# Kernel optimization log

Hardware: AMD Instinct MI355X
Metric: run time of the kernel (lower is better)

## Reference

```python
import jax, jax.numpy as jnp
import numpy as np

D_MODEL = 256
N_HEAD = 8


def quick_gelu(x):
    return x * jax.nn.sigmoid(1.702 * x)


def setup_inputs() -> dict:
    key = jax.random.key(0)
    ks = jax.random.split(key, 7)
    d = D_MODEL
    s = 0.02
    return {
        "x": jax.random.normal(ks[0], (2, 512, d), dtype=jnp.float32),
        "W_qkv": jax.random.normal(ks[1], (d, 3 * d), dtype=jnp.float32) * s,
        "b_qkv": jnp.zeros((3 * d,), dtype=jnp.float32),
        "W_fc": jax.random.normal(ks[2], (d, 4 * d), dtype=jnp.float32) * s,
        "b_fc": jnp.zeros((4 * d,), dtype=jnp.float32),
        "W_proj": jax.random.normal(ks[3], (4 * d, d), dtype=jnp.float32) * s,
        "b_proj": jnp.zeros((d,), dtype=jnp.float32),
    }


def attention_l1(x, W_qkv, b_qkv):
    bs, n_ctx, width = x.shape
    h = N_HEAD
    c = width // h
    scale = 1.0 / jnp.sqrt(jnp.asarray(c, x.dtype))
    qkv = (x @ W_qkv + b_qkv).reshape(bs, n_ctx, h, 3 * c)
    q, k, v = jnp.split(qkv, 3, axis=-1)  # each (b, t, h, c)
    qh = q.transpose(0, 2, 1, 3)  # (b, h, t, c)
    kh = k.transpose(0, 2, 1, 3)  # (b, h, s, c)
    vh = v.transpose(0, 2, 1, 3)  # (b, h, s, c)
    # L1 distance: sum_c |q - k| * scale  -> (b, h, t, s)
    dist = jnp.sum(jnp.abs(qh[:, :, :, None, :] - kh[:, :, None, :, :]), axis=-1) * scale
    weight = 1.0 / (0.001 + dist)
    idx = jnp.arange(n_ctx)
    weight = weight.at[:, :, idx, idx].set(0.0)
    wdtype = weight.dtype
    weight = jax.nn.softmax(weight.astype(jnp.float32), axis=-1).astype(wdtype)
    out = jnp.einsum('bhts,bhsc->bthc', weight, vh)
    return out.reshape(bs, n_ctx, width)


def reference(x, W_qkv, b_qkv, W_fc, b_fc, W_proj, b_proj):
    x = x + attention_l1(x, W_qkv, b_qkv)
    h = quick_gelu(x @ W_fc + b_fc)
    x = x + (h @ W_proj + b_proj)
    return x
```

## Files before the change

kernel.cpp:

```cpp
#include <hip/hip_runtime.h>
#include <hip/hip_bf16.h>

#define DM   256
#define NH   8
#define HC   32
#define SEQ  512
#define BATCH 2
#define MTOT (BATCH*SEQ)

#define OFF_Q    0
#define OFF_K    262144
#define OFF_X1   524288
#define FP32_END 786432
#define BOFF_XB     0
#define BOFF_X1B    262144
#define BOFF_HB     524288
#define BOFF_VTB    1572864
#define BOFF_WQKVT  1835008
#define BOFF_WFCT   2031616
#define BOFF_WPROJT 2293760

typedef __attribute__((ext_vector_type(8))) __bf16 bf16x8;
typedef __attribute__((ext_vector_type(4))) __bf16 bf16x4;
typedef __attribute__((ext_vector_type(4))) float  f32x4;

__device__ __forceinline__ float qgelu(float x) {
    return x / (1.0f + __expf(-1.702f * x));
}

__device__ __forceinline__ void conv_copy(const float* __restrict__ in,
                                          __bf16* __restrict__ out,
                                          int total, int gid) {
    int o = gid * 4;
    if (o >= total) return;
    float4 v = *(const float4*)(in + o);
    bf16x4 b;
    b.x = (__bf16)v.x; b.y = (__bf16)v.y; b.z = (__bf16)v.z; b.w = (__bf16)v.w;
    *(bf16x4*)(out + o) = b;
}

__device__ __forceinline__ void conv_transpose(const float* __restrict__ in,
                                               __bf16* __restrict__ out,
                                               int K, int N, int gid) {
    int o = gid * 4;
    if (o >= K * N) return;
    int n = o / K;
    int k = o - n * K;
    bf16x4 b;
    b.x = (__bf16)in[(size_t)(k + 0) * N + n];
    b.y = (__bf16)in[(size_t)(k + 1) * N + n];
    b.z = (__bf16)in[(size_t)(k + 2) * N + n];
    b.w = (__bf16)in[(size_t)(k + 3) * N + n];
    *(bf16x4*)(out + o) = b;
}

__global__ __launch_bounds__(256)
void convert_k(const float* __restrict__ x,
               const float* __restrict__ Wqkv,
               const float* __restrict__ Wfc,
               const float* __restrict__ Wproj,
               __bf16* __restrict__ wsb)
{
    const int gid = blockIdx.x * 256 + threadIdx.x;
    switch (blockIdx.y) {
        case 0: conv_copy(x, wsb + BOFF_XB, MTOT * DM, gid); break;
        case 1: conv_transpose(Wqkv,  wsb + BOFF_WQKVT,  256, 768,  gid); break;
        case 2: conv_transpose(Wfc,   wsb + BOFF_WFCT,   256, 1024, gid); break;
        case 3: conv_transpose(Wproj, wsb + BOFF_WPROJT, 1024, 256, gid); break;
    }
}

template<int MODE, int K_>
__global__ __launch_bounds__(256)
void mfma_gemm(const __bf16* __restrict__ A, const __bf16* __restrict__ Bt,
               const float* __restrict__ bias, const float* __restrict__ X1res,
               float* __restrict__ Of, __bf16* __restrict__ Ob,
               float* __restrict__ ws, __bf16* __restrict__ vtb, int N)
{
    const int lane = threadIdx.x & 63;
    const int wv   = threadIdx.x >> 6;
    const int m0   = blockIdx.y * 16;
    const int n0   = blockIdx.x * 64 + wv * 16;
    const int r    = lane & 15;
    const int q    = lane >> 4;

    const __bf16* ap = A  + (size_t)(m0 + r) * K_ + q * 8;
    const __bf16* bp = Bt + (size_t)(n0 + r) * K_ + q * 8;

    f32x4 acc = {0.f, 0.f, 0.f, 0.f};
    #pragma unroll
    for (int kt = 0; kt < K_; kt += 32) {
        bf16x8 af = *(const bf16x8*)(ap + kt);
        bf16x8 bf = *(const bf16x8*)(bp + kt);
        acc = __builtin_amdgcn_mfma_f32_16x16x32_bf16(af, bf, acc, 0, 0, 0);
    }

    const int n = n0 + r;
    const float bn = bias[n];
    #pragma unroll
    for (int i = 0; i < 4; ++i) {
        const int m = m0 + q * 4 + i;
        float v = acc[i] + bn;
        if (MODE == 0) {
            const int b  = m >> 9, t = m & 511;
            const int h  = n / 96, jj = n % 96;
            const int bh = b * NH + h;
            if (jj < 32)      ws[OFF_Q + ((size_t)(bh * SEQ + t)) * HC + jj]        = v;
            else if (jj < 64) ws[OFF_K + ((size_t)(bh * SEQ + t)) * HC + (jj - 32)] = v;
            else              vtb[((size_t)(bh * HC + (jj - 64))) * SEQ + t] = (__bf16)v;
        } else if (MODE == 1) {
            Ob[(size_t)m * N + n] = (__bf16)qgelu(v);
        } else {
            Of[(size_t)m * N + n] = X1res[(size_t)m * N + n] + v;
        }
    }
}

#define QT 16
#define PSTRIDE 514

__global__ __launch_bounds__(512, 4)
void attn_k(const float* __restrict__ wq, const float* __restrict__ wk,
            const __bf16* __restrict__ vtb, const float* __restrict__ xin,
            float* __restrict__ x1, __bf16* __restrict__ x1b)
{
    __shared__ float  qtile[QT * 32];
    __shared__ __bf16 pmat[QT * PSTRIDE];
    __shared__ float  psum[QT * 8];
    __shared__ float  pinv[QT];

    const int tid  = threadIdx.x;
    const int lane = tid & 63;
    const int wv   = tid >> 6;
    const int sg   = tid;
    const int bh   = blockIdx.x >> 5;
    const int qbase = (blockIdx.x & 31) * QT;
    const float scale = 0.17677669529663687f;

    const float* krow = wk + ((size_t)(bh * SEQ + sg)) * HC;
    float kr[32];
    #pragma unroll
    for (int j = 0; j < 8; ++j) {
        float4 k4 = *(const float4*)&krow[j * 4];
        kr[j*4+0] = k4.x; kr[j*4+1] = k4.y; kr[j*4+2] = k4.z; kr[j*4+3] = k4.w;
    }
    if (tid < QT * 32 / 4) {
        *(float4*)&qtile[tid * 4] =
            *(const float4*)&wq[((size_t)(bh * SEQ + qbase)) * HC + tid * 4];
    }
    __syncthreads();

    #pragma unroll 4
    for (int t = 0; t < QT; ++t) {
        float d = 0.f;
        #pragma unroll
        for (int j = 0; j < 8; ++j) {
            float4 q4 = *(const float4*)&qtile[t * 32 + j * 4];
            d += fabsf(kr[j*4+0] - q4.x) + fabsf(kr[j*4+1] - q4.y)
               + fabsf(kr[j*4+2] - q4.z) + fabsf(kr[j*4+3] - q4.w);
        }
        float w = 1.0f / (0.001f + d * scale);
        if (sg == qbase + t) w = 0.0f;
        float p = __expf(w);
        float se = p;
        #pragma unroll
        for (int off = 32; off >= 1; off >>= 1) se += __shfl_xor(se, off, 64);
        pmat[t * PSTRIDE + sg] = (__bf16)p;
        if (lane == 0) psum[t * 8 + wv] = se;
    }
    __syncthreads();

    if (tid < QT) {
        float s = 0.f;
        #pragma unroll
        for (int j = 0; j < 8; ++j) s += psum[tid * 8 + j];
        pinv[tid] = 1.0f / s;
    }
    __syncthreads();

    if (wv < 2) {
        const int r = lane & 15, q = lane >> 4;
        const __bf16* bp  = vtb + ((size_t)(bh * HC + wv * 16 + r)) * SEQ + q * 8;
        const __bf16* apm = &pmat[r * PSTRIDE + q * 8];

        f32x4 acc = {0.f, 0.f, 0.f, 0.f};
        #pragma unroll
        for (int kt = 0; kt < SEQ; kt += 32) {
            bf16x8 af = *(const bf16x8*)(apm + kt);
            bf16x8 bf = *(const bf16x8*)(bp + kt);
            acc = __builtin_amdgcn_mfma_f32_16x16x32_bf16(af, bf, acc, 0, 0, 0);
        }

        const int b = bh >> 3, hh = bh & 7;
        const int c = wv * 16 + r;
        #pragma unroll
        for (int i = 0; i < 4; ++i) {
            const int tl = q * 4 + i;
            const int t  = qbase + tl;
            const float v = acc[i] * pinv[tl];
            const int idx = ((b * SEQ + t) * DM) + hh * HC + c;
            const float res = xin[idx] + v;
            x1[idx]  = res;
            x1b[idx] = (__bf16)res;
        }
    }
}

extern "C" void kernel_launch(void* const* d_in, const int* in_sizes, int n_in,
                              void* d_out, int out_size, void* d_ws, size_t ws_size,
                              hipStream_t stream)
{
    (void)in_sizes; (void)n_in; (void)out_size; (void)ws_size;
    const float* x     = (const float*)d_in[0];
    const float* Wqkv  = (const float*)d_in[1];
    const float* bqkv  = (const float*)d_in[2];
    const float* Wfc   = (const float*)d_in[3];
    const float* bfc   = (const float*)d_in[4];
    const float* Wproj = (const float*)d_in[5];
    const float* bproj = (const float*)d_in[6];
    float* out = (float*)d_out;
    float* ws  = (float*)d_ws;
    __bf16* wsb = (__bf16*)(ws + FP32_END);

    convert_k<<<dim3(256, 4), 256, 0, stream>>>(x, Wqkv, Wfc, Wproj, wsb);

    mfma_gemm<0, 256><<<dim3(768/64, MTOT/16), 256, 0, stream>>>(
        wsb + BOFF_XB, wsb + BOFF_WQKVT, bqkv, nullptr,
        nullptr, nullptr, ws, wsb + BOFF_VTB, 768);

    attn_k<<<dim3(512), 512, 0, stream>>>(
        ws + OFF_Q, ws + OFF_K, wsb + BOFF_VTB, x, ws + OFF_X1, wsb + BOFF_X1B);

    mfma_gemm<1, 256><<<dim3(1024/64, MTOT/16), 256, 0, stream>>>(
        wsb + BOFF_X1B, wsb + BOFF_WFCT, bfc, nullptr,
        nullptr, wsb + BOFF_HB, ws, nullptr, 1024);

    mfma_gemm<2, 1024><<<dim3(256/64, MTOT/16), 256, 0, stream>>>(
        wsb + BOFF_HB, wsb + BOFF_WPROJT, bproj, ws + OFF_X1,
        out, nullptr, ws, nullptr, 256);
}
```

Baseline: 116.8 us.

## Fuse all stages into one cooperative persistent kernel with grid syncs

Replaces the five separate launches (convert, QKV GEMM, attention, FC GEMM, proj GEMM) with a single cooperative kernel of 256 blocks of 1024 threads, separated by grid.sync barriers. Weight transposes now go through an LDS tile for coalesced access. Attention processes 32 query rows per block. The proj GEMM is split along K into four parts and reduced in LDS. This removes launch gaps and tail effects at the cost of grid-wide barriers and a fixed grid size, which may limit occupancy.

```diff
diff --git a/kernel.cpp b/kernel.cpp
--- a/kernel.cpp
+++ b/kernel.cpp
@@ -1,12 +1,14 @@
 #include <hip/hip_runtime.h>
 #include <hip/hip_bf16.h>
+#include <hip/hip_cooperative_groups.h>
+
+namespace cg = cooperative_groups;
 
 #define DM   256
 #define NH   8
 #define HC   32
 #define SEQ  512
-#define BATCH 2
-#define MTOT (BATCH*SEQ)
+#define MTOT 1024
 
 #define OFF_Q    0
 #define OFF_K    262144
@@ -24,69 +26,23 @@
 typedef __attribute__((ext_vector_type(4))) __bf16 bf16x4;
 typedef __attribute__((ext_vector_type(4))) float  f32x4;
 
+#define QT 32
+#define PSTRIDE 514
+
 __device__ __forceinline__ float qgelu(float x) {
     return x / (1.0f + __expf(-1.702f * x));
 }
 
-__device__ __forceinline__ void conv_copy(const float* __restrict__ in,
-                                          __bf16* __restrict__ out,
-                                          int total, int gid) {
-    int o = gid * 4;
-    if (o >= total) return;
-    float4 v = *(const float4*)(in + o);
-    bf16x4 b;
-    b.x = (__bf16)v.x; b.y = (__bf16)v.y; b.z = (__bf16)v.z; b.w = (__bf16)v.w;
-    *(bf16x4*)(out + o) = b;
-}
-
-__device__ __forceinline__ void conv_transpose(const float* __restrict__ in,
-                                               __bf16* __restrict__ out,
-                                               int K, int N, int gid) {
-    int o = gid * 4;
-    if (o >= K * N) return;
-    int n = o / K;
-    int k = o - n * K;
-    bf16x4 b;
-    b.x = (__bf16)in[(size_t)(k + 0) * N + n];
-    b.y = (__bf16)in[(size_t)(k + 1) * N + n];
-    b.z = (__bf16)in[(size_t)(k + 2) * N + n];
-    b.w = (__bf16)in[(size_t)(k + 3) * N + n];
-    *(bf16x4*)(out + o) = b;
-}
-
-__global__ __launch_bounds__(256)
-void convert_k(const float* __restrict__ x,
-               const float* __restrict__ Wqkv,
-               const float* __restrict__ Wfc,
-               const float* __restrict__ Wproj,
-               __bf16* __restrict__ wsb)
+template<int MODE, int K_>
+__device__ __forceinline__ void gemm_tile16(
+    const __bf16* __restrict__ A, const __bf16* __restrict__ Bt,
+    const float* __restrict__ bias,
+    __bf16* __restrict__ Ob, float* __restrict__ ws, __bf16* __restrict__ vtb,
+    int m0, int n0, int N, int lane)
 {
-    const int gid = blockIdx.x * 256 + threadIdx.x;
-    switch (blockIdx.y) {
-        case 0: conv_copy(x, wsb + BOFF_XB, MTOT * DM, gid); break;
-        case 1: conv_transpose(Wqkv,  wsb + BOFF_WQKVT,  256, 768,  gid); break;
-        case 2: conv_transpose(Wfc,   wsb + BOFF_WFCT,   256, 1024, gid); break;
-        case 3: conv_transpose(Wproj, wsb + BOFF_WPROJT, 1024, 256, gid); break;
-    }
-}
-
-template<int MODE, int K_>
-__global__ __launch_bounds__(256)
-void mfma_gemm(const __bf16* __restrict__ A, const __bf16* __restrict__ Bt,
-               const float* __restrict__ bias, const float* __restrict__ X1res,
-               float* __restrict__ Of, __bf16* __restrict__ Ob,
-               float* __restrict__ ws, __bf16* __restrict__ vtb, int N)
-{
-    const int lane = threadIdx.x & 63;
-    const int wv   = threadIdx.x >> 6;
-    const int m0   = blockIdx.y * 16;
-    const int n0   = blockIdx.x * 64 + wv * 16;
-    const int r    = lane & 15;
-    const int q    = lane >> 4;
-
+    const int r = lane & 15, q = lane >> 4;
     const __bf16* ap = A  + (size_t)(m0 + r) * K_ + q * 8;
     const __bf16* bp = Bt + (size_t)(n0 + r) * K_ + q * 8;
-
     f32x4 acc = {0.f, 0.f, 0.f, 0.f};
     #pragma unroll
     for (int kt = 0; kt < K_; kt += 32) {
@@ -94,7 +50,6 @@
         bf16x8 bf = *(const bf16x8*)(bp + kt);
         acc = __builtin_amdgcn_mfma_f32_16x16x32_bf16(af, bf, acc, 0, 0, 0);
     }
-
     const int n = n0 + r;
     const float bn = bias[n];
     #pragma unroll
@@ -108,100 +63,190 @@
             if (jj < 32)      ws[OFF_Q + ((size_t)(bh * SEQ + t)) * HC + jj]        = v;
             else if (jj < 64) ws[OFF_K + ((size_t)(bh * SEQ + t)) * HC + (jj - 32)] = v;
             else              vtb[((size_t)(bh * HC + (jj - 64))) * SEQ + t] = (__bf16)v;
-        } else if (MODE == 1) {
+        } else {
             Ob[(size_t)m * N + n] = (__bf16)qgelu(v);
-        } else {
-            Of[(size_t)m * N + n] = X1res[(size_t)m * N + n] + v;
-        }
-    }
-}
-
-#define QT 16
-#define PSTRIDE 514
-
-__global__ __launch_bounds__(512, 4)
-void attn_k(const float* __restrict__ wq, const float* __restrict__ wk,
-            const __bf16* __restrict__ vtb, const float* __restrict__ xin,
-            float* __restrict__ x1, __bf16* __restrict__ x1b)
+        }
+    }
+}
+
+__global__ __launch_bounds__(1024, 4)
+void fused_k(const float* __restrict__ x,
+             const float* __restrict__ Wqkv, const float* __restrict__ bqkv,
+             const float* __restrict__ Wfc,  const float* __restrict__ bfc,
+             const float* __restrict__ Wproj,const float* __restrict__ bproj,
+             float* __restrict__ out, float* __restrict__ ws)
 {
-    __shared__ float  qtile[QT * 32];
-    __shared__ __bf16 pmat[QT * PSTRIDE];
-    __shared__ float  psum[QT * 8];
-    __shared__ float  pinv[QT];
-
+    __shared__ __align__(16) float smem[9600];
+    __bf16* wsb = (__bf16*)(ws + FP32_END);
     const int tid  = threadIdx.x;
+    const int bid  = blockIdx.x;
     const int lane = tid & 63;
     const int wv   = tid >> 6;
-    const int sg   = tid;
-    const int bh   = blockIdx.x >> 5;
-    const int qbase = (blockIdx.x & 31) * QT;
-    const float scale = 0.17677669529663687f;
-
-    const float* krow = wk + ((size_t)(bh * SEQ + sg)) * HC;
-    float kr[32];
-    #pragma unroll
-    for (int j = 0; j < 8; ++j) {
-        float4 k4 = *(const float4*)&krow[j * 4];
-        kr[j*4+0] = k4.x; kr[j*4+1] = k4.y; kr[j*4+2] = k4.z; kr[j*4+3] = k4.w;
-    }
-    if (tid < QT * 32 / 4) {
-        *(float4*)&qtile[tid * 4] =
-            *(const float4*)&wq[((size_t)(bh * SEQ + qbase)) * HC + tid * 4];
-    }
-    __syncthreads();
-
-    #pragma unroll 4
-    for (int t = 0; t < QT; ++t) {
-        float d = 0.f;
+    cg::grid_group grid = cg::this_grid();
+
+    if (bid >= 176) {
+        int gid = (bid - 176) * 1024 + tid;
+        if (gid < MTOT * DM / 4) {
+            float4 v = *(const float4*)(x + gid * 4);
+            bf16x4 b;
+            b.x = (__bf16)v.x; b.y = (__bf16)v.y; b.z = (__bf16)v.z; b.w = (__bf16)v.w;
+            *(bf16x4*)(wsb + BOFF_XB + gid * 4) = b;
+        }
+    } else {
+        const float* src; __bf16* dst; int K, N, tile;
+        if (bid < 48)       { src = Wqkv;  dst = wsb + BOFF_WQKVT;  K = 256;  N = 768;  tile = bid; }
+        else if (bid < 112) { src = Wfc;   dst = wsb + BOFF_WFCT;   K = 256;  N = 1024; tile = bid - 48; }
+        else                { src = Wproj; dst = wsb + BOFF_WPROJT; K = 1024; N = 256;  tile = bid - 112; }
+        const int nn = N >> 6;
+        const int k0 = (tile / nn) * 64, n0 = (tile % nn) * 64;
+        float* lt = smem;
+        const int rr = tid >> 4, c4 = tid & 15;
+        float4 v = *(const float4*)&src[(size_t)(k0 + rr) * N + n0 + c4 * 4];
+        lt[rr * 65 + c4 * 4 + 0] = v.x; lt[rr * 65 + c4 * 4 + 1] = v.y;
+        lt[rr * 65 + c4 * 4 + 2] = v.z; lt[rr * 65 + c4 * 4 + 3] = v.w;
+        __syncthreads();
+        bf16x4 b;
+        b.x = (__bf16)lt[(c4 * 4 + 0) * 65 + rr];
+        b.y = (__bf16)lt[(c4 * 4 + 1) * 65 + rr];
+        b.z = (__bf16)lt[(c4 * 4 + 2) * 65 + rr];
+        b.w = (__bf16)lt[(c4 * 4 + 3) * 65 + rr];
+        *(bf16x4*)&dst[(size_t)(n0 + rr) * K + k0 + c4 * 4] = b;
+    }
+    grid.sync();
+
+    {
+        const int widx = bid * 16 + wv;
+        if (widx < 3072) {
+            const int mt = widx & 63, nt = widx >> 6;
+            gemm_tile16<0, 256>(wsb + BOFF_XB, wsb + BOFF_WQKVT, bqkv,
+                                nullptr, ws, wsb + BOFF_VTB,
+                                mt * 16, nt * 16, 768, lane);
+        }
+    }
+    grid.sync();
+
+    {
+        float*  qtile = smem;
+        __bf16* pmat  = (__bf16*)(smem + 1024);
+        float*  psum  = smem + 1024 + (QT * PSTRIDE) / 2;
+        float*  pinv  = psum + QT * 8;
+        const int bh    = bid >> 4;
+        const int qbase = (bid & 15) * QT;
+        const int hf    = tid >> 9;
+        const int sg    = tid & 511;
+        const float scale = 0.17677669529663687f;
+
+        const float* krow = ws + OFF_K + ((size_t)(bh * SEQ + sg)) * HC;
+        float kr[32];
         #pragma unroll
         for (int j = 0; j < 8; ++j) {
-            float4 q4 = *(const float4*)&qtile[t * 32 + j * 4];
-            d += fabsf(kr[j*4+0] - q4.x) + fabsf(kr[j*4+1] - q4.y)
-               + fabsf(kr[j*4+2] - q4.z) + fabsf(kr[j*4+3] - q4.w);
-        }
-        float w = 1.0f / (0.001f + d * scale);
-        if (sg == qbase + t) w = 0.0f;
-        float p = __expf(w);
-        float se = p;
-        #pragma unroll
-        for (int off = 32; off >= 1; off >>= 1) se += __shfl_xor(se, off, 64);
-        pmat[t * PSTRIDE + sg] = (__bf16)p;
-        if (lane == 0) psum[t * 8 + wv] = se;
-    }
-    __syncthreads();
-
-    if (tid < QT) {
-        float s = 0.f;
-        #pragma unroll
-        for (int j = 0; j < 8; ++j) s += psum[tid * 8 + j];
-        pinv[tid] = 1.0f / s;
-    }
-    __syncthreads();
-
-    if (wv < 2) {
+            float4 k4 = *(const float4*)&krow[j * 4];
+            kr[j*4+0] = k4.x; kr[j*4+1] = k4.y; kr[j*4+2] = k4.z; kr[j*4+3] = k4.w;
+        }
+        if (tid < 256) {
+            *(float4*)&qtile[tid * 4] =
+                *(const float4*)&ws[OFF_Q + ((size_t)(bh * SEQ + qbase)) * HC + tid * 4];
+        }
+        __syncthreads();
+
+        #pragma unroll 4
+        for (int tl = 0; tl < 16; ++tl) {
+            const int trow = hf * 16 + tl;
+            float d = 0.f;
+            #pragma unroll
+            for (int j = 0; j < 8; ++j) {
+                float4 q4 = *(const float4*)&qtile[trow * 32 + j * 4];
+                d += fabsf(kr[j*4+0] - q4.x) + fabsf(kr[j*4+1] - q4.y)
+                   + fabsf(kr[j*4+2] - q4.z) + fabsf(kr[j*4+3] - q4.w);
+            }
+            float w = 1.0f / (0.001f + d * scale);
+            if (sg == qbase + trow) w = 0.0f;
+            float p = __expf(w);
+            float se = p;
+            #pragma unroll
+            for (int off = 32; off >= 1; off >>= 1) se += __shfl_xor(se, off, 64);
+            pmat[trow * PSTRIDE + sg] = (__bf16)p;
+            if (lane == 0) psum[trow * 8 + (wv & 7)] = se;
+        }
+        __syncthreads();
+        if (tid < QT) {
+            float s = 0.f;
+            #pragma unroll
+            for (int j = 0; j < 8; ++j) s += psum[tid * 8 + j];
+            pinv[tid] = 1.0f / s;
+        }
+        __syncthreads();
+
+        if (wv < 4) {
+            const int r = lane & 15, q = lane >> 4;
+            const int qtl = wv >> 1, ctl = wv & 1;
+            const __bf16* apm = &pmat[(qtl * 16 + r) * PSTRIDE + q * 8];
+            const __bf16* bp  = wsb + BOFF_VTB +
+                                ((size_t)(bh * HC + ctl * 16 + r)) * SEQ + q * 8;
+            f32x4 acc = {0.f, 0.f, 0.f, 0.f};
+            #pragma unroll
+            for (int kt = 0; kt < SEQ; kt += 32) {
+                bf16x8 af = *(const bf16x8*)(apm + kt);
+                bf16x8 bf = *(const bf16x8*)(bp + kt);
+                acc = __builtin_amdgcn_mfma_f32_16x16x32_bf16(af, bf, acc, 0, 0, 0);
+            }
+            const int b = bh >> 3, hh = bh & 7;
+            const int c = ctl * 16 + r;
+            #pragma unroll
+            for (int i = 0; i < 4; ++i) {
+                const int trow = qtl * 16 + q * 4 + i;
+                const int t    = qbase + trow;
+                const float v  = acc[i] * pinv[trow];
+                const int idx  = ((b * SEQ + t) * DM) + hh * HC + c;
+                const float res = x[idx] + v;
+                ws[OFF_X1 + idx]    = res;
+                wsb[BOFF_X1B + idx] = (__bf16)res;
+            }
+        }
+    }
+    grid.sync();
+
+    {
+        const int widx = bid * 16 + wv;
+        const int mt = widx & 63, nt = widx >> 6;
+        gemm_tile16<1, 256>(wsb + BOFF_X1B, wsb + BOFF_WFCT, bfc,
+                            wsb + BOFF_HB, ws, nullptr,
+                            mt * 16, nt * 16, 1024, lane);
+    }
+    grid.sync();
+
+    {
+        float* ared = smem;
+        const int widx = bid * 16 + wv;
+        const int tile = widx >> 2, ks = widx & 3;
+        const int m0 = (tile & 63) * 16, n0 = (tile >> 6) * 16;
         const int r = lane & 15, q = lane >> 4;
-        const __bf16* bp  = vtb + ((size_t)(bh * HC + wv * 16 + r)) * SEQ + q * 8;
-        const __bf16* apm = &pmat[r * PSTRIDE + q * 8];
-
+        const __bf16* ap = wsb + BOFF_HB     + (size_t)(m0 + r) * 1024 + ks * 256 + q * 8;
+        const __bf16* bp = wsb + BOFF_WPROJT + (size_t)(n0 + r) * 1024 + ks * 256 + q * 8;
         f32x4 acc = {0.f, 0.f, 0.f, 0.f};
         #pragma unroll
-        for (int kt = 0; kt < SEQ; kt += 32) {
-            bf16x8 af = *(const bf16x8*)(apm + kt);
-            bf16x8 bf = *(const bf16x8*)(bp + kt);
+        for (int kk = 0; kk < 8; ++kk) {
+            bf16x8 af = *(const bf16x8*)(ap + kk * 32);
+            bf16x8 bf = *(const bf16x8*)(bp + kk * 32);
             acc = __builtin_amdgcn_mfma_f32_16x16x32_bf16(af, bf, acc, 0, 0, 0);
         }
-
-        const int b = bh >> 3, hh = bh & 7;
-        const int c = wv * 16 + r;
-        #pragma unroll
-        for (int i = 0; i < 4; ++i) {
-            const int tl = q * 4 + i;
-            const int t  = qbase + tl;
-            const float v = acc[i] * pinv[tl];
-            const int idx = ((b * SEQ + t) * DM) + hh * HC + c;
-            const float res = xin[idx] + v;
-            x1[idx]  = res;
-            x1b[idx] = (__bf16)res;
+        *(f32x4*)&ared[(wv * 64 + lane) * 4] = acc;
+        __syncthreads();
+        if (wv < 4) {
+            const int tile2 = bid * 4 + wv;
+            const int m0b = (tile2 & 63) * 16, n0b = (tile2 >> 6) * 16;
+            f32x4 a0 = *(const f32x4*)&ared[((wv * 4 + 0) * 64 + lane) * 4];
+            f32x4 a1 = *(const f32x4*)&ared[((wv * 4 + 1) * 64 + lane) * 4];
+            f32x4 a2 = *(const f32x4*)&ared[((wv * 4 + 2) * 64 + lane) * 4];
+            f32x4 a3 = *(const f32x4*)&ared[((wv * 4 + 3) * 64 + lane) * 4];
+            const int n = n0b + r;
+            const float bn = bproj[n];
+            #pragma unroll
+            for (int i = 0; i < 4; ++i) {
+                const int m = m0b + q * 4 + i;
+                const float v = a0[i] + a1[i] + a2[i] + a3[i] + bn;
+                out[(size_t)m * DM + n] = ws[OFF_X1 + (size_t)m * DM + n] + v;
+            }
         }
     }
 }
@@ -220,22 +265,10 @@
     const float* bproj = (const float*)d_in[6];
     float* out = (float*)d_out;
     float* ws  = (float*)d_ws;
-    __bf16* wsb = (__bf16*)(ws + FP32_END);
-
-    convert_k<<<dim3(256, 4), 256, 0, stream>>>(x, Wqkv, Wfc, Wproj, wsb);
-
-    mfma_gemm<0, 256><<<dim3(768/64, MTOT/16), 256, 0, stream>>>(
-        wsb + BOFF_XB, wsb + BOFF_WQKVT, bqkv, nullptr,
-        nullptr, nullptr, ws, wsb + BOFF_VTB, 768);
-
-    attn_k<<<dim3(512), 512, 0, stream>>>(
-        ws + OFF_Q, ws + OFF_K, wsb + BOFF_VTB, x, ws + OFF_X1, wsb + BOFF_X1B);
-
-    mfma_gemm<1, 256><<<dim3(1024/64, MTOT/16), 256, 0, stream>>>(
-        wsb + BOFF_X1B, wsb + BOFF_WFCT, bfc, nullptr,
-        nullptr, wsb + BOFF_HB, ws, nullptr, 1024);
-
-    mfma_gemm<2, 1024><<<dim3(256/64, MTOT/16), 256, 0, stream>>>(
-        wsb + BOFF_HB, wsb + BOFF_WPROJT, bproj, ws + OFF_X1,
-        out, nullptr, ws, nullptr, 256);
-}
+
+    void* args[] = { (void*)&x, (void*)&Wqkv, (void*)&bqkv, (void*)&Wfc,
+                     (void*)&bfc, (void*)&Wproj, (void*)&bproj,
+                     (void*)&out, (void*)&ws };
+    hipLaunchCooperativeKernel((const void*)fused_k, dim3(256), dim3(1024),
+                               args, 0, stream);
+}
```

New measurement: 256.3 us. 2.2x slower.

## Restructure GEMM kernels: LDS-tiled weight transpose, fused x conversion, split-K projection

Applied to the files above, without the earlier changes.

Replaces the strided-gather weight conversion with an LDS-tiled transpose kernel that reads and writes coalesced. The x fp32-to-bf16 copy is folded into the QKV GEMM, which now converts on load. The GEMMs get their own kernels with a one-wave-per-16x16-tile mapping, ordered so that consecutive waves share B rows. The projection GEMM (K=1024) is split into four K slices across waves and reduced through LDS, giving more blocks and shorter serial MFMA chains. The cost is an extra LDS reduction and sync in the projection kernel.

```diff
diff --git a/kernel.cpp b/kernel.cpp
--- a/kernel.cpp
+++ b/kernel.cpp
@@ -5,14 +5,12 @@
 #define NH   8
 #define HC   32
 #define SEQ  512
-#define BATCH 2
-#define MTOT (BATCH*SEQ)
+#define MTOT 1024
 
 #define OFF_Q    0
 #define OFF_K    262144
 #define OFF_X1   524288
 #define FP32_END 786432
-#define BOFF_XB     0
 #define BOFF_X1B    262144
 #define BOFF_HB     524288
 #define BOFF_VTB    1572864
@@ -28,91 +26,76 @@
     return x / (1.0f + __expf(-1.702f * x));
 }
 
-__device__ __forceinline__ void conv_copy(const float* __restrict__ in,
-                                          __bf16* __restrict__ out,
-                                          int total, int gid) {
-    int o = gid * 4;
-    if (o >= total) return;
-    float4 v = *(const float4*)(in + o);
-    bf16x4 b;
-    b.x = (__bf16)v.x; b.y = (__bf16)v.y; b.z = (__bf16)v.z; b.w = (__bf16)v.w;
-    *(bf16x4*)(out + o) = b;
-}
-
-__device__ __forceinline__ void conv_transpose(const float* __restrict__ in,
-                                               __bf16* __restrict__ out,
-                                               int K, int N, int gid) {
-    int o = gid * 4;
-    if (o >= K * N) return;
-    int n = o / K;
-    int k = o - n * K;
-    bf16x4 b;
-    b.x = (__bf16)in[(size_t)(k + 0) * N + n];
-    b.y = (__bf16)in[(size_t)(k + 1) * N + n];
-    b.z = (__bf16)in[(size_t)(k + 2) * N + n];
-    b.w = (__bf16)in[(size_t)(k + 3) * N + n];
-    *(bf16x4*)(out + o) = b;
-}
-
-__global__ __launch_bounds__(256)
-void convert_k(const float* __restrict__ x,
-               const float* __restrict__ Wqkv,
-               const float* __restrict__ Wfc,
-               const float* __restrict__ Wproj,
-               __bf16* __restrict__ wsb)
-{
-    const int gid = blockIdx.x * 256 + threadIdx.x;
-    switch (blockIdx.y) {
-        case 0: conv_copy(x, wsb + BOFF_XB, MTOT * DM, gid); break;
-        case 1: conv_transpose(Wqkv,  wsb + BOFF_WQKVT,  256, 768,  gid); break;
-        case 2: conv_transpose(Wfc,   wsb + BOFF_WFCT,   256, 1024, gid); break;
-        case 3: conv_transpose(Wproj, wsb + BOFF_WPROJT, 1024, 256, gid); break;
-    }
-}
-
-template<int MODE, int K_>
-__global__ __launch_bounds__(256)
-void mfma_gemm(const __bf16* __restrict__ A, const __bf16* __restrict__ Bt,
-               const float* __restrict__ bias, const float* __restrict__ X1res,
-               float* __restrict__ Of, __bf16* __restrict__ Ob,
-               float* __restrict__ ws, __bf16* __restrict__ vtb, int N)
-{
-    const int lane = threadIdx.x & 63;
-    const int wv   = threadIdx.x >> 6;
-    const int m0   = blockIdx.y * 16;
-    const int n0   = blockIdx.x * 64 + wv * 16;
-    const int r    = lane & 15;
-    const int q    = lane >> 4;
-
-    const __bf16* ap = A  + (size_t)(m0 + r) * K_ + q * 8;
-    const __bf16* bp = Bt + (size_t)(n0 + r) * K_ + q * 8;
+__global__ __launch_bounds__(256)
+void trans_k(const float* __restrict__ Wqkv, const float* __restrict__ Wfc,
+             const float* __restrict__ Wproj, __bf16* __restrict__ wsb)
+{
+    __shared__ float lt[64 * 65];
+    const int bid = blockIdx.x, tid = threadIdx.x;
+    const float* src; __bf16* dst; int K, N, tile;
+    if (bid < 48)       { src = Wqkv;  dst = wsb + BOFF_WQKVT;  K = 256;  N = 768;  tile = bid; }
+    else if (bid < 112) { src = Wfc;   dst = wsb + BOFF_WFCT;   K = 256;  N = 1024; tile = bid - 48; }
+    else                { src = Wproj; dst = wsb + BOFF_WPROJT; K = 1024; N = 256;  tile = bid - 112; }
+    const int nn = N >> 6;
+    const int k0 = (tile / nn) * 64, n0 = (tile % nn) * 64;
+    const int rr0 = tid >> 4, c4 = tid & 15;
+    #pragma unroll
+    for (int i = 0; i < 4; ++i) {
+        const int rr = rr0 + i * 16;
+        float4 v = *(const float4*)&src[(size_t)(k0 + rr) * N + n0 + c4 * 4];
+        lt[rr * 65 + c4 * 4 + 0] = v.x; lt[rr * 65 + c4 * 4 + 1] = v.y;
+        lt[rr * 65 + c4 * 4 + 2] = v.z; lt[rr * 65 + c4 * 4 + 3] = v.w;
+    }
+    __syncthreads();
+    #pragma unroll
+    for (int i = 0; i < 4; ++i) {
+        const int rr = rr0 + i * 16;
+        bf16x4 b;
+        b.x = (__bf16)lt[(c4 * 4 + 0) * 65 + rr];
+        b.y = (__bf16)lt[(c4 * 4 + 1) * 65 + rr];
+        b.z = (__bf16)lt[(c4 * 4 + 2) * 65 + rr];
+        b.w = (__bf16)lt[(c4 * 4 + 3) * 65 + rr];
+        *(bf16x4*)&dst[(size_t)(n0 + rr) * K + k0 + c4 * 4] = b;
+    }
+}
+
+__global__ __launch_bounds__(256)
+void qkv_k(const float* __restrict__ x, const __bf16* __restrict__ Bt,
+           const float* __restrict__ bias, float* __restrict__ ws,
+           __bf16* __restrict__ vtb)
+{
+    const int lane = threadIdx.x & 63, wv = threadIdx.x >> 6;
+    const int widx = blockIdx.x * 4 + wv;
+    const int m0 = (widx & 63) * 16, n0 = (widx >> 6) * 16;
+    const int r = lane & 15, q = lane >> 4;
+
+    const float*  ap = x  + (size_t)(m0 + r) * DM + q * 8;
+    const __bf16* bp = Bt + (size_t)(n0 + r) * DM + q * 8;
 
     f32x4 acc = {0.f, 0.f, 0.f, 0.f};
     #pragma unroll
-    for (int kt = 0; kt < K_; kt += 32) {
-        bf16x8 af = *(const bf16x8*)(ap + kt);
+    for (int kt = 0; kt < DM; kt += 32) {
+        float4 a0 = *(const float4*)(ap + kt);
+        float4 a1 = *(const float4*)(ap + kt + 4);
+        bf16x8 af;
+        af[0] = (__bf16)a0.x; af[1] = (__bf16)a0.y; af[2] = (__bf16)a0.z; af[3] = (__bf16)a0.w;
+        af[4] = (__bf16)a1.x; af[5] = (__bf16)a1.y; af[6] = (__bf16)a1.z; af[7] = (__bf16)a1.w;
         bf16x8 bf = *(const bf16x8*)(bp + kt);
         acc = __builtin_amdgcn_mfma_f32_16x16x32_bf16(af, bf, acc, 0, 0, 0);
     }
 
     const int n = n0 + r;
     const float bn = bias[n];
+    const int h = n / 96, jj = n % 96;
     #pragma unroll
     for (int i = 0; i < 4; ++i) {
         const int m = m0 + q * 4 + i;
-        float v = acc[i] + bn;
-        if (MODE == 0) {
-            const int b  = m >> 9, t = m & 511;
-            const int h  = n / 96, jj = n % 96;
-            const int bh = b * NH + h;
-            if (jj < 32)      ws[OFF_Q + ((size_t)(bh * SEQ + t)) * HC + jj]        = v;
-            else if (jj < 64) ws[OFF_K + ((size_t)(bh * SEQ + t)) * HC + (jj - 32)] = v;
-            else              vtb[((size_t)(bh * HC + (jj - 64))) * SEQ + t] = (__bf16)v;
-        } else if (MODE == 1) {
-            Ob[(size_t)m * N + n] = (__bf16)qgelu(v);
-        } else {
-            Of[(size_t)m * N + n] = X1res[(size_t)m * N + n] + v;
-        }
+        const float v = acc[i] + bn;
+        const int b = m >> 9, t = m & 511;
+        const int bh = b * NH + h;
+        if (jj < 32)      ws[OFF_Q + ((size_t)(bh * SEQ + t)) * HC + jj]        = v;
+        else if (jj < 64) ws[OFF_K + ((size_t)(bh * SEQ + t)) * HC + (jj - 32)] = v;
+        else              vtb[((size_t)(bh * HC + (jj - 64))) * SEQ + t] = (__bf16)v;
     }
 }
 
@@ -182,7 +165,6 @@
         const int r = lane & 15, q = lane >> 4;
         const __bf16* bp  = vtb + ((size_t)(bh * HC + wv * 16 + r)) * SEQ + q * 8;
         const __bf16* apm = &pmat[r * PSTRIDE + q * 8];
-
         f32x4 acc = {0.f, 0.f, 0.f, 0.f};
         #pragma unroll
         for (int kt = 0; kt < SEQ; kt += 32) {
@@ -190,7 +172,6 @@
             bf16x8 bf = *(const bf16x8*)(bp + kt);
             acc = __builtin_amdgcn_mfma_f32_16x16x32_bf16(af, bf, acc, 0, 0, 0);
         }
-
         const int b = bh >> 3, hh = bh & 7;
         const int c = wv * 16 + r;
         #pragma unroll
@@ -202,6 +183,73 @@
             const float res = xin[idx] + v;
             x1[idx]  = res;
             x1b[idx] = (__bf16)res;
+        }
+    }
+}
+
+__global__ __launch_bounds__(256)
+void fc_k(const __bf16* __restrict__ A, const __bf16* __restrict__ Bt,
+          const float* __restrict__ bias, __bf16* __restrict__ Ob)
+{
+    const int lane = threadIdx.x & 63, wv = threadIdx.x >> 6;
+    const int widx = blockIdx.x * 4 + wv;
+    const int m0 = (widx & 63) * 16, n0 = (widx >> 6) * 16;
+    const int r = lane & 15, q = lane >> 4;
+
+    const __bf16* ap = A  + (size_t)(m0 + r) * DM + q * 8;
+    const __bf16* bp = Bt + (size_t)(n0 + r) * DM + q * 8;
+
+    f32x4 acc = {0.f, 0.f, 0.f, 0.f};
+    #pragma unroll
+    for (int kt = 0; kt < DM; kt += 32) {
+        bf16x8 af = *(const bf16x8*)(ap + kt);
+        bf16x8 bf = *(const bf16x8*)(bp + kt);
+        acc = __builtin_amdgcn_mfma_f32_16x16x32_bf16(af, bf, acc, 0, 0, 0);
+    }
+
+    const int n = n0 + r;
+    const float bn = bias[n];
+    #pragma unroll
+    for (int i = 0; i < 4; ++i) {
+        const int m = m0 + q * 4 + i;
+        Ob[(size_t)m * 1024 + n] = (__bf16)qgelu(acc[i] + bn);
+    }
+}
+
+__global__ __launch_bounds__(256)
+void proj_k(const __bf16* __restrict__ H, const __bf16* __restrict__ Bt,
+            const float* __restrict__ bias, const float* __restrict__ X1,
+            float* __restrict__ out)
+{
+    __shared__ f32x4 ared[4][64];
+    const int lane = threadIdx.x & 63, wv = threadIdx.x >> 6;
+    const int tile = blockIdx.x;
+    const int m0 = (tile & 63) * 16, n0 = (tile >> 6) * 16;
+    const int r = lane & 15, q = lane >> 4;
+
+    const __bf16* ap = H  + (size_t)(m0 + r) * 1024 + wv * 256 + q * 8;
+    const __bf16* bp = Bt + (size_t)(n0 + r) * 1024 + wv * 256 + q * 8;
+
+    f32x4 acc = {0.f, 0.f, 0.f, 0.f};
+    #pragma unroll
+    for (int kk = 0; kk < 8; ++kk) {
+        bf16x8 af = *(const bf16x8*)(ap + kk * 32);
+        bf16x8 bf = *(const bf16x8*)(bp + kk * 32);
+        acc = __builtin_amdgcn_mfma_f32_16x16x32_bf16(af, bf, acc, 0, 0, 0);
+    }
+    ared[wv][lane] = acc;
+    __syncthreads();
+
+    if (wv == 0) {
+        f32x4 a0 = ared[0][lane], a1 = ared[1][lane];
+        f32x4 a2 = ared[2][lane], a3 = ared[3][lane];
+        const int n = n0 + r;
+        const float bn = bias[n];
+        #pragma unroll
+        for (int i = 0; i < 4; ++i) {
+            const int m = m0 + q * 4 + i;
+            const float v = a0[i] + a1[i] + a2[i] + a3[i] + bn;
+            out[(size_t)m * DM + n] = X1[(size_t)m * DM + n] + v;
         }
     }
 }
@@ -222,20 +270,16 @@
     float* ws  = (float*)d_ws;
     __bf16* wsb = (__bf16*)(ws + FP32_END);
 
-    convert_k<<<dim3(256, 4), 256, 0, stream>>>(x, Wqkv, Wfc, Wproj, wsb);
-
-    mfma_gemm<0, 256><<<dim3(768/64, MTOT/16), 256, 0, stream>>>(
-        wsb + BOFF_XB, wsb + BOFF_WQKVT, bqkv, nullptr,
-        nullptr, nullptr, ws, wsb + BOFF_VTB, 768);
-
-    attn_k<<<dim3(512), 512, 0, stream>>>(
-        ws + OFF_Q, ws + OFF_K, wsb + BOFF_VTB, x, ws + OFF_X1, wsb + BOFF_X1B);
-
-    mfma_gemm<1, 256><<<dim3(1024/64, MTOT/16), 256, 0, stream>>>(
-        wsb + BOFF_X1B, wsb + BOFF_WFCT, bfc, nullptr,
-        nullptr, wsb + BOFF_HB, ws, nullptr, 1024);
-
-    mfma_gemm<2, 1024><<<dim3(256/64, MTOT/16), 256, 0, stream>>>(
-        wsb + BOFF_HB, wsb + BOFF_WPROJT, bproj, ws + OFF_X1,
-        out, nullptr, ws, nullptr, 256);
-}
+    trans_k<<<176, 256, 0, stream>>>(Wqkv, Wfc, Wproj, wsb);
+
+    qkv_k<<<768, 256, 0, stream>>>(x, wsb + BOFF_WQKVT, bqkv, ws, wsb + BOFF_VTB);
+
+    attn_k<<<512, 512, 0, stream>>>(ws + OFF_Q, ws + OFF_K, wsb + BOFF_VTB,
+                                    x, ws + OFF_X1, wsb + BOFF_X1B);
+
+    fc_k<<<1024, 256, 0, stream>>>(wsb + BOFF_X1B, wsb + BOFF_WFCT, bfc,
+                                   wsb + BOFF_HB);
+
+    proj_k<<<1024, 256, 0, stream>>>(wsb + BOFF_HB, wsb + BOFF_WPROJT, bproj,
+                                     ws + OFF_X1, out);
+}
```

Result: no change. 117.6 us (+0.7%).
